# Kernel optimization log

Hardware: AMD Instinct MI355X
Metric: run time of the kernel (lower is better)

## Reference

```python
import jax, jax.numpy as jnp
import numpy as np

C, D, K, N, R = 96, 192, 4, 16, 6  # d_model, d_inner, directions, d_state, dt_rank
B, H, W = 8, 64, 64


def _ln(x, w, b):
    mu = x.mean(-1, keepdims=True)
    var = ((x - mu) ** 2).mean(-1, keepdims=True)
    return (x - mu) * jax.lax.rsqrt(var + 1e-5) * w + b


def setup_inputs() -> dict:
    key = jax.random.key(0)
    ks = jax.random.split(key, 16)
    s = 0.02
    A = jnp.tile(jnp.arange(1, N + 1, dtype=jnp.float32)[None, None, :], (K, D, 1))
    return {
        "x": jax.random.normal(ks[0], (B, C, H, W), jnp.float32),
        "ln1_w": jnp.ones((C,), jnp.float32),
        "ln1_b": jnp.zeros((C,), jnp.float32),
        "in_proj_w": jax.random.normal(ks[1], (2 * D, C), jnp.float32) * s,
        "conv_w": jax.random.normal(ks[2], (D, 1, 3, 3), jnp.float32) * s,
        "conv_b": jnp.zeros((D,), jnp.float32),
        "x_proj_w": jax.random.normal(ks[3], (K, R + 2 * N, D), jnp.float32) * s,
        "dt_projs_w": jax.random.normal(ks[4], (K, D, R), jnp.float32) * s,
        "dt_projs_b": jax.random.normal(ks[5], (K, D), jnp.float32) * 0.1,
        "A_logs": jnp.log(A),
        "Ds": jnp.ones((K, D), jnp.float32),
        "out_norm_w": jnp.ones((D,), jnp.float32),
        "out_norm_b": jnp.zeros((D,), jnp.float32),
        "out_proj_w": jax.random.normal(ks[6], (C, D), jnp.float32) * s,
        "pm_norm_w": jnp.ones((4 * C,), jnp.float32),
        "pm_norm_b": jnp.zeros((4 * C,), jnp.float32),
        "pm_red_w": jax.random.normal(ks[7], (2 * C, 4 * C), jnp.float32) * s,
    }


def reference(x, ln1_w, ln1_b, in_proj_w, conv_w, conv_b, x_proj_w, dt_projs_w,
              dt_projs_b, A_logs, Ds, out_norm_w, out_norm_b, out_proj_w,
              pm_norm_w, pm_norm_b, pm_red_w):
    b, c, h, w = x.shape
    L = h * w
    xh = jnp.transpose(x, (0, 2, 3, 1))  # [B,H,W,C]
    resid = xh
    xn = _ln(xh, ln1_w, ln1_b)
    xz = xn @ in_proj_w.T  # [B,H,W,2D]
    xp, z = xz[..., :D], xz[..., D:]
    xc = jnp.transpose(xp, (0, 3, 1, 2))  # [B,D,H,W]
    xc = jax.lax.conv_general_dilated(
        xc, conv_w, (1, 1), ((1, 1), (1, 1)),
        dimension_numbers=("NCHW", "OIHW", "NCHW"), feature_group_count=D)
    xc = jax.nn.silu(xc + conv_b[None, :, None, None])
    # cross-scan: row-major, col-major, and their reverses -> [B,K,D,L]
    xf = xc.reshape(b, D, L)
    xt = jnp.transpose(xc, (0, 1, 3, 2)).reshape(b, D, L)
    xs = jnp.stack([xf, xt, xf[..., ::-1], xt[..., ::-1]], axis=1)
    x_dbl = jnp.einsum("bkdl,kcd->bkcl", xs, x_proj_w)
    dts = jnp.einsum("bkrl,kdr->bkdl", x_dbl[:, :, :R], dt_projs_w)
    Bs = x_dbl[:, :, R:R + N]  # [B,K,N,L]
    Cs = x_dbl[:, :, R + N:R + 2 * N]
    delta = jax.nn.softplus(dts + dt_projs_b[None, :, :, None])  # [B,K,D,L]
    A = -jnp.exp(A_logs)  # [K,D,N]
    dT = jnp.transpose(delta, (3, 0, 1, 2))  # [L,B,K,D]
    uT = jnp.transpose(xs, (3, 0, 1, 2))
    BT = jnp.transpose(Bs, (3, 0, 1, 2))  # [L,B,K,N]
    CT = jnp.transpose(Cs, (3, 0, 1, 2))
    h0 = jnp.zeros((b, K, D, N), x.dtype)

    def step(hst, inp):
        dt, ut, bt, ct = inp
        hst = hst * jnp.exp(dt[..., None] * A) + (dt * ut)[..., None] * bt[:, :, None, :]
        return hst, jnp.einsum("bkdn,bkn->bkd", hst, ct)

    _, yT = jax.lax.scan(step, h0, (dT, uT, BT, CT))  # yT: [L,B,K,D]
    y = jnp.transpose(yT, (1, 2, 3, 0)) + Ds[None, :, :, None] * xs  # [B,K,D,L]

    def unT(v):  # undo col-major traversal
        return jnp.transpose(v.reshape(b, D, w, h), (0, 1, 3, 2)).reshape(b, D, L)

    yc = y[:, 0] + y[:, 2, :, ::-1] + unT(y[:, 1]) + unT(y[:, 3, :, ::-1])
    yo = jnp.transpose(yc.reshape(b, D, h, w), (0, 2, 3, 1))  # [B,H,W,D]
    yo = _ln(yo, out_norm_w, out_norm_b) * jax.nn.silu(z)
    out = resid + yo @ out_proj_w.T  # [B,H,W,C]
    # PatchMerging2D
    x0 = out[:, 0::2, 0::2]
    x1 = out[:, 1::2, 0::2]
    x2 = out[:, 0::2, 1::2]
    x3 = out[:, 1::2, 1::2]
    xm = jnp.concatenate([x0, x1, x2, x3], -1)  # [B,H/2,W/2,4C]
    xm = _ln(xm, pm_norm_w, pm_norm_b) @ pm_red_w.T  # [B,H/2,W/2,2C]
    return jnp.transpose(xm, (0, 3, 1, 2))
```

## Files before the change

### kernel.cpp

```cpp
#include <hip/hip_runtime.h>
#include <hip/hip_bf16.h>


#define NCH 64
#define CLEN 64

typedef float v2f __attribute__((ext_vector_type(2)));
__device__ __forceinline__ v2f pkfma(v2f a, v2f b, v2f c){ return __builtin_elementwise_fma(a,b,c); }

__device__ __forceinline__ float sigm(float x){ return 1.f/(1.f+__expf(-x)); }
__device__ __forceinline__ float softplus_(float x){ return (x>20.f)? x : __logf(1.f+__expf(x)); }

__device__ __forceinline__ unsigned packbf2(float a, float b){
  __hip_bfloat16 ba = __float2bfloat16(a), bb = __float2bfloat16(b);
  unsigned short ua = *(unsigned short*)&ba, ub = *(unsigned short*)&bb;
  return (unsigned)ua | ((unsigned)ub<<16);
}
__device__ __forceinline__ float unpk_lo(unsigned u){ return __uint_as_float((u&0xffffu)<<16); }
__device__ __forceinline__ float unpk_hi(unsigned u){ return __uint_as_float(u&0xffff0000u); }

__device__ __forceinline__ void scan_p0dp2(int k, int v0, int& p0, int& dp){
  if(k==0){ p0 = v0; dp = 1; }
  else if(k==1){ p0 = ((v0&63)<<6)|(v0>>6); dp = 64; }
  else if(k==2){ p0 = 4095 - v0; dp = -1; }
  else { int m0 = 4095 - v0; p0 = ((m0&63)<<6)|(m0>>6); dp = -64; }
}

__global__ __launch_bounds__(256) void k0_prep(
    const float* __restrict__ ipw, const float* __restrict__ xpw,
    const float* __restrict__ dtw, const float* __restrict__ opw,
    const float* __restrict__ pmw,
    float* __restrict__ ipwT, float* __restrict__ xpwTp,
    float* __restrict__ dtwT, float* __restrict__ opwT,
    float* __restrict__ pmwT)
{
  int g = blockIdx.x*256 + threadIdx.x;
  if(g < 36864){
    int c = g/384, n = g%384;
    ipwT[g] = ipw[n*96 + c];
  } else if(g < 67584){
    int t = g - 36864; int dd = t/160, n = t - dd*160; int k = n/40, c = n - k*40;
    float v;
    if(c < 6)       v = xpw[(k*38 + c)*192 + dd];
    else if(c < 8)  v = 0.f;
    else            v = xpw[(k*38 + (c-2))*192 + dd];
    xpwTp[t] = v;
  } else if(g < 72192){
    int t = g - 67584; int kr = t/192, d = t - kr*192; int k = kr/6, r = kr - k*6;
    dtwT[t] = dtw[(k*192 + d)*6 + r];
  } else if(g < 90624){
    int t = g - 72192; int d = t/96, c = t - d*96;
    opwT[t] = opw[c*192 + d];
  } else if(g < 164352){
    int t = g - 90624; int n = t/192, c2 = t - n*192;
    pmwT[t] = pmw[c2*384 + n];
  }
}

#define XT_PAD 68
__global__ __launch_bounds__(256) void k1_ln_inproj(
    const float* __restrict__ x, const float* __restrict__ lnw, const float* __restrict__ lnb,
    const float* __restrict__ ipwT, float* __restrict__ xT,
    float* __restrict__ xp, float* __restrict__ z)
{
  __shared__ float xt[96*XT_PAD];
  __shared__ float lnw_s[96], lnb_s[96], mu_s[64], rs_s[64];
  int tid = threadIdx.x;
  int mt = blockIdx.x, nt = blockIdx.y, b = blockIdx.z;
  int g0 = mt*64;
  const float* xb = x + (size_t)b*96*4096 + g0;
  for(int idx=tid; idx<6144; idx+=256){
    int c = idx>>6, p = idx&63;
    xt[c*XT_PAD+p] = xb[c*4096 + p];
  }
  if(tid<96){ lnw_s[tid]=lnw[tid]; lnb_s[tid]=lnb[tid]; }
  __syncthreads();
  if(nt==0){
    float* xTb = xT + ((size_t)(b*4096 + g0))*96;
    for(int idx=tid; idx<6144; idx+=256){
      int p = idx/96, c = idx - p*96;
      xTb[idx] = xt[c*XT_PAD+p];
    }
  }
  if(tid<64){
    float s=0.f,q=0.f;
    for(int c=0;c<96;c++){ float v=xt[c*XT_PAD+tid]; s+=v; q+=v*v; }
    float mu = s*(1.f/96.f);
    mu_s[tid]=mu; rs_s[tid]=rsqrtf(q*(1.f/96.f)-mu*mu+1e-5f);
  }
  __syncthreads();
  for(int idx=tid; idx<6144; idx+=256){
    int c = idx>>6, p = idx&63;
    int a = c*XT_PAD+p;
    xt[a] = (xt[a]-mu_s[p])*rs_s[p]*lnw_s[c]+lnb_s[c];
  }
  __syncthreads();
  int tm = tid>>5, tn = tid&31;
  float acc[8][4];
  #pragma unroll
  for(int i=0;i<8;i++){acc[i][0]=0.f;acc[i][1]=0.f;acc[i][2]=0.f;acc[i][3]=0.f;}
  const float* wbase = ipwT + nt*128 + tn*4;
  for(int kk=0;kk<96;kk++){
    float4 w4 = *(const float4*)(wbase + kk*384);
    float4 a0 = *(const float4*)&xt[kk*XT_PAD + tm*8];
    float4 a1 = *(const float4*)&xt[kk*XT_PAD + tm*8 + 4];
    float av[8]={a0.x,a0.y,a0.z,a0.w,a1.x,a1.y,a1.z,a1.w};
    #pragma unroll
    for(int i=0;i<8;i++){
      acc[i][0]=fmaf(av[i],w4.x,acc[i][0]);
      acc[i][1]=fmaf(av[i],w4.y,acc[i][1]);
      acc[i][2]=fmaf(av[i],w4.z,acc[i][2]);
      acc[i][3]=fmaf(av[i],w4.w,acc[i][3]);
    }
  }
  int n = nt*128 + tn*4;
  #pragma unroll
  for(int i=0;i<8;i++){
    size_t row = (size_t)(b*4096 + g0 + tm*8 + i);
    float4 v = make_float4(acc[i][0],acc[i][1],acc[i][2],acc[i][3]);
    if(n < 192) *(float4*)(xp + row*192 + n) = v;
    else        *(float4*)(z  + row*192 + (n-192)) = v;
  }
}

__global__ __launch_bounds__(192) void k2_conv(
    const float* __restrict__ xp, const float* __restrict__ cw, const float* __restrict__ cb,
    __hip_bfloat16* __restrict__ xc)
{
  __shared__ float cw_s[1728];
  int tid = threadIdx.x;
  int pq = blockIdx.x, b = blockIdx.y;
  for(int i=tid;i<1728;i+=192) cw_s[i]=cw[i];
  __syncthreads();
  int th = (pq>>3)<<1;
  int tw = (pq&7)<<3;
  const float* base = xp + (size_t)b*4096*192 + tid;
  const float* wp = &cw_s[tid*9];
  float bias = cb[tid];
  float acc[2][8];
  #pragma unroll
  for(int r=0;r<2;r++)
    #pragma unroll
    for(int j=0;j<8;j++) acc[r][j]=bias;
  #pragma unroll
  for(int iy=0; iy<4; iy++){
    int hh = th-1+iy;
    if(hh<0||hh>63) continue;
    float v[10];
    #pragma unroll
    for(int xx=0;xx<10;xx++){
      int ww = tw-1+xx;
      v[xx] = (ww>=0 && ww<64) ? base[((size_t)(hh*64+ww))*192] : 0.f;
    }
    #pragma unroll
    for(int r=0;r<2;r++){
      int ky = iy - r;
      if(ky<0||ky>2) continue;
      float wk0=wp[ky*3], wk1=wp[ky*3+1], wk2=wp[ky*3+2];
      #pragma unroll
      for(int j=0;j<8;j++)
        acc[r][j] = fmaf(v[j],wk0, fmaf(v[j+1],wk1, fmaf(v[j+2],wk2, acc[r][j])));
    }
  }
  #pragma unroll
  for(int r=0;r<2;r++)
    #pragma unroll
    for(int j=0;j<8;j++){
      float a = acc[r][j];
      a = a * sigm(a);
      xc[((size_t)(b*4096) + (th+r)*64 + tw+j)*192 + tid] = __float2bfloat16(a);
    }
}

__global__ __launch_bounds__(320) void k3_proj(
    const __hip_bfloat16* __restrict__ xc, const float* __restrict__ xpwTp,
    float* __restrict__ xdbl)
{
  __shared__ float sm[32*192];
  int tid = threadIdx.x;
  int mt = blockIdx.x, b = blockIdx.y;
  int g0 = mt*32;
  const unsigned* xcb = (const unsigned*)(xc + ((size_t)(b*4096 + g0))*192);
  for(int idx=tid; idx<3072; idx+=320){
    unsigned u = xcb[idx];
    sm[idx*2]   = unpk_lo(u);
    sm[idx*2+1] = unpk_hi(u);
  }
  __syncthreads();
  int tn = tid%40, tm = tid/40;
  float acc[4][4];
  #pragma unroll
  for(int i=0;i<4;i++){acc[i][0]=0.f;acc[i][1]=0.f;acc[i][2]=0.f;acc[i][3]=0.f;}
  const float* wb = xpwTp + tn*4;
  for(int kk=0;kk<192;kk+=2){
    float4 w0 = *(const float4*)(wb + kk*160);
    float4 w1 = *(const float4*)(wb + (kk+1)*160);
    #pragma unroll
    for(int i=0;i<4;i++){
      float2 a = *(const float2*)&sm[(tm*4+i)*192 + kk];
      acc[i][0] = fmaf(a.x,w0.x, fmaf(a.y,w1.x, acc[i][0]));
      acc[i][1] = fmaf(a.x,w0.y, fmaf(a.y,w1.y, acc[i][1]));
      acc[i][2] = fmaf(a.x,w0.z, fmaf(a.y,w1.z, acc[i][2]));
      acc[i][3] = fmaf(a.x,w0.w, fmaf(a.y,w1.w, acc[i][3]));
    }
  }
  #pragma unroll
  for(int i=0;i<4;i++){
    *(float4*)(xdbl + ((size_t)(b*4096 + g0 + tm*4 + i))*160 + tn*4)
      = make_float4(acc[i][0],acc[i][1],acc[i][2],acc[i][3]);
  }
}

__global__ __launch_bounds__(192) void k4a_scanlocal(
    const float* __restrict__ xdbl, const __hip_bfloat16* __restrict__ xc,
    const float* __restrict__ alog, const float* __restrict__ dtwT,
    const float* __restrict__ dtb,
    __hip_bfloat16* __restrict__ localH, float* __restrict__ Ssum)
{
  int d = threadIdx.x;
  int ch = blockIdx.x, k = blockIdx.y, b = blockIdx.z;
  size_t prow = (size_t)b*4096;
  int p0, dp;
  scan_p0dp2(k, ch*CLEN, p0, dp);
  const float* rowp = xdbl + (prow + (size_t)p0)*160 + k*40;
  ptrdiff_t rstride = (ptrdiff_t)dp*160;
  float w0=dtwT[(k*6+0)*192+d], w1=dtwT[(k*6+1)*192+d], w2=dtwT[(k*6+2)*192+d],
        w3=dtwT[(k*6+3)*192+d], w4=dtwT[(k*6+4)*192+d], w5=dtwT[(k*6+5)*192+d];
  float dtbv = dtb[k*192+d];
  float A0; bool fast1;
  {
    const float4* ap = (const float4*)(alog + (size_t)(k*192+d)*16);
    float4 a0=ap[0],a1=ap[1],a2=ap[2],a3=ap[3];
    float t[16]={a0.x,a0.y,a0.z,a0.w,a1.x,a1.y,a1.z,a1.w,a2.x,a2.y,a2.z,a2.w,a3.x,a3.y,a3.z,a3.w};
    A0 = -__expf(t[0]);
    bool fast = true;
    #pragma unroll
    for(int n=1;n<16;n++)
      fast = fast && (fabsf(-__expf(t[n]) - (float)(n+1)*A0) <= 1e-4f*(float)(n+1)*fabsf(A0));
    fast1 = fast && (A0 == -1.0f);
  }
  float S=0.f;
  const __hip_bfloat16* xu = xc + (prow + (size_t)p0)*192 + d;
  ptrdiff_t ustride = (ptrdiff_t)dp*192;
  unsigned* lh = (unsigned*)(localH + ((((size_t)(b*4+k))*NCH + ch)*192 + d)*16);
  if(fast1){
    v2f h01={0.f,0.f},h23={0.f,0.f},h45={0.f,0.f},h67={0.f,0.f},
        h89={0.f,0.f},hAB={0.f,0.f},hCD={0.f,0.f},hEF={0.f,0.f};
    for(int i=0;i<CLEN;i++){
      const float* row = rowp; rowp += rstride;
      float u = __bfloat162float(*xu); xu += ustride;
      float4 r03 = *(const float4*)row;
      float2 r45 = *(const float2*)(row+4);
      float p01 = fmaf(r03.y,w1, r03.x*w0);
      float p23 = fmaf(r03.w,w3, r03.z*w2);
      float p45 = fmaf(r45.y,w5, r45.x*w4);
      float raw = (dtbv + p01) + (p23 + p45);
      float ex = __expf(raw);
      float tt = 1.f + ex;
      float delta = (raw>20.f)? raw : __logf(tt);
      float e1 = __builtin_amdgcn_rcpf(tt);
      float du = delta*u;
      S += delta;
      float4 B0=*(const float4*)(row+8),  B1=*(const float4*)(row+12),
             B2=*(const float4*)(row+16), B3=*(const float4*)(row+20);
      float e2s = e1*e1;
      v2f e2v = {e2s,e2s};
      v2f e4v = e2v*e2v;
      v2f e8v = e4v*e4v;
      v2f c01 = {e1,e2s};
      v2f c23 = c01*e2v;
      v2f c45 = c01*e4v;
      v2f c67 = c23*e4v;
      v2f c89 = c01*e8v;
      v2f cAB = c23*e8v;
      v2f cCD = c45*e8v;
      v2f cEF = c67*e8v;
      v2f du2 = {du,du};
      h01 = pkfma(h01,c01, du2*(v2f){B0.x,B0.y});
      h23 = pkfma(h23,c23, du2*(v2f){B0.z,B0.w});
      h45 = pkfma(h45,c45, du2*(v2f){B1.x,B1.y});
      h67 = pkfma(h67,c67, du2*(v2f){B1.z,B1.w});
      h89 = pkfma(h89,c89, du2*(v2f){B2.x,B2.y});
      hAB = pkfma(hAB,cAB, du2*(v2f){B2.z,B2.w});
      hCD = pkfma(hCD,cCD, du2*(v2f){B3.x,B3.y});
      hEF = pkfma(hEF,cEF, du2*(v2f){B3.z,B3.w});
    }
    uint4 q0, q1;
    q0.x = packbf2(h01.x,h01.y); q0.y = packbf2(h23.x,h23.y);
    q0.z = packbf2(h45.x,h45.y); q0.w = packbf2(h67.x,h67.y);
    q1.x = packbf2(h89.x,h89.y); q1.y = packbf2(hAB.x,hAB.y);
    q1.z = packbf2(hCD.x,hCD.y); q1.w = packbf2(hEF.x,hEF.y);
    *(uint4*)lh = q0;
    *(uint4*)(lh+4) = q1;
  } else {
    float A[16], h[16];
    {
      const float4* ap = (const float4*)(alog + (size_t)(k*192+d)*16);
      float4 a0=ap[0],a1=ap[1],a2=ap[2],a3=ap[3];
      float t[16]={a0.x,a0.y,a0.z,a0.w,a1.x,a1.y,a1.z,a1.w,a2.x,a2.y,a2.z,a2.w,a3.x,a3.y,a3.z,a3.w};
      #pragma unroll
      for(int n=0;n<16;n++){ A[n] = -__expf(t[n]); h[n]=0.f; }
    }
    for(int i=0;i<CLEN;i++){
      const float* row = rowp; rowp += rstride;
      float u = __bfloat162float(*xu); xu += ustride;
      float p01 = fmaf(row[1],w1, row[0]*w0);
      float p23 = fmaf(row[3],w3, row[2]*w2);
      float p45 = fmaf(row[5],w5, row[4]*w4);
      float delta = softplus_((dtbv + p01) + (p23 + p45));
      float du = delta*u;
      S += delta;
      float4 B0=*(const float4*)(row+8),  B1=*(const float4*)(row+12),
             B2=*(const float4*)(row+16), B3=*(const float4*)(row+20);
      float Bn[16]={B0.x,B0.y,B0.z,B0.w,B1.x,B1.y,B1.z,B1.w,
                    B2.x,B2.y,B2.z,B2.w,B3.x,B3.y,B3.z,B3.w};
      #pragma unroll
      for(int n=0;n<16;n++) h[n] = fmaf(h[n], __expf(delta*A[n]), du*Bn[n]);
    }
    uint4 q0, q1;
    q0.x = packbf2(h[0],h[1]);   q0.y = packbf2(h[2],h[3]);
    q0.z = packbf2(h[4],h[5]);   q0.w = packbf2(h[6],h[7]);
    q1.x = packbf2(h[8],h[9]);   q1.y = packbf2(h[10],h[11]);
    q1.z = packbf2(h[12],h[13]); q1.w = packbf2(h[14],h[15]);
    *(uint4*)lh = q0;
    *(uint4*)(lh+4) = q1;
  }
  Ssum[(((size_t)(b*4+k))*NCH + ch)*192 + d] = S;
}

__global__ __launch_bounds__(256) void k4b_chain(
    __hip_bfloat16* __restrict__ localH, const float* __restrict__ Ssum,
    const float* __restrict__ alog)
{
  int g = blockIdx.x*256 + threadIdx.x;
  int bk = g/3072, dn = g - bk*3072;
  int k = bk & 3;
  int d = dn>>4, n = dn&15;
  float A = -__expf(alog[((size_t)(k*192+d))*16 + n]);
  size_t hbase = (size_t)bk*NCH*3072 + dn;
  size_t sbase = (size_t)bk*NCH*192 + d;
  float hv = 0.f;
  float loc = __bfloat162float(localH[hbase]);
  float S   = Ssum[sbase];
  for(int ch=0; ch<NCH; ch++){
    float nloc = 0.f, nS = 0.f;
    if(ch < NCH-1){
      nloc = __bfloat162float(localH[hbase + (size_t)(ch+1)*3072]);
      nS   = Ssum[sbase + (size_t)(ch+1)*192];
    }
    float dec = __expf(A*S);
    localH[hbase + (size_t)ch*3072] = __float2bfloat16(hv);
    hv = fmaf(hv, dec, loc);
    loc = nloc; S = nS;
  }
}

__global__ __launch_bounds__(192) void k4c_scanfull(
    const float* __restrict__ xdbl, const __hip_bfloat16* __restrict__ xc,
    const float* __restrict__ alog, const float* __restrict__ dtwT,
    const float* __restrict__ dtb, const __hip_bfloat16* __restrict__ hin,
    const float* __restrict__ Dsv, __hip_bfloat16* __restrict__ yB)
{
  int d = threadIdx.x;
  int ch = blockIdx.x, k = blockIdx.y, b = blockIdx.z;
  size_t prow = (size_t)b*4096;
  int p0, dp;
  scan_p0dp2(k, ch*CLEN, p0, dp);
  const float* rowp = xdbl + (prow + (size_t)p0)*160 + k*40;
  ptrdiff_t rstride = (ptrdiff_t)dp*160;
  float w0=dtwT[(k*6+0)*192+d], w1=dtwT[(k*6+1)*192+d], w2=dtwT[(k*6+2)*192+d],
        w3=dtwT[(k*6+3)*192+d], w4=dtwT[(k*6+4)*192+d], w5=dtwT[(k*6+5)*192+d];
  float dtbv = dtb[k*192+d];
  float A0; bool fast1;
  {
    const float4* ap = (const float4*)(alog + (size_t)(k*192+d)*16);
    float4 a0=ap[0],a1=ap[1],a2=ap[2],a3=ap[3];
    float t[16]={a0.x,a0.y,a0.z,a0.w,a1.x,a1.y,a1.z,a1.w,a2.x,a2.y,a2.z,a2.w,a3.x,a3.y,a3.z,a3.w};
    A0 = -__expf(t[0]);
    bool fast = true;
    #pragma unroll
    for(int n=1;n<16;n++)
      fast = fast && (fabsf(-__expf(t[n]) - (float)(n+1)*A0) <= 1e-4f*(float)(n+1)*fabsf(A0));
    fast1 = fast && (A0 == -1.0f);
  }
  float dsv = Dsv[k*192+d];
  const __hip_bfloat16* xu = xc + (prow + (size_t)p0)*192 + d;
  ptrdiff_t ustride = (ptrdiff_t)dp*192;
  __hip_bfloat16* yP = yB + (((size_t)(b*4+k))*4096 + ch*CLEN)*192 + d;
  const unsigned* hp = (const unsigned*)(hin + ((((size_t)(b*4+k))*NCH + ch)*192 + d)*16);
  uint4 q0 = *(const uint4*)hp;
  uint4 q1 = *(const uint4*)(hp+4);
  if(fast1){
    v2f h01={unpk_lo(q0.x),unpk_hi(q0.x)}, h23={unpk_lo(q0.y),unpk_hi(q0.y)},
        h45={unpk_lo(q0.z),unpk_hi(q0.z)}, h67={unpk_lo(q0.w),unpk_hi(q0.w)},
        h89={unpk_lo(q1.x),unpk_hi(q1.x)}, hAB={unpk_lo(q1.y),unpk_hi(q1.y)},
        hCD={unpk_lo(q1.z),unpk_hi(q1.z)}, hEF={unpk_lo(q1.w),unpk_hi(q1.w)};
    for(int i=0;i<CLEN;i++){
      const float* row = rowp; rowp += rstride;
      float u = __bfloat162float(*xu); xu += ustride;
      float4 r03 = *(const float4*)row;
      float2 r45 = *(const float2*)(row+4);
      float p01 = fmaf(r03.y,w1, r03.x*w0);
      float p23 = fmaf(r03.w,w3, r03.z*w2);
      float p45 = fmaf(r45.y,w5, r45.x*w4);
      float raw = (dtbv + p01) + (p23 + p45);
      float ex = __expf(raw);
      float tt = 1.f + ex;
      float delta = (raw>20.f)? raw : __logf(tt);
      float e1 = __builtin_amdgcn_rcpf(tt);
      float du = delta*u;
      float4 B0=*(const float4*)(row+8),  B1=*(const float4*)(row+12),
             B2=*(const float4*)(row+16), B3=*(const float4*)(row+20);
      float4 C0=*(const float4*)(row+24), C1=*(const float4*)(row+28),
             C2=*(const float4*)(row+32), C3=*(const float4*)(row+36);
      float e2s = e1*e1;
      v2f e2v = {e2s,e2s};
      v2f e4v = e2v*e2v;
      v2f e8v = e4v*e4v;
      v2f c01 = {e1,e2s};
      v2f c23 = c01*e2v;
      v2f c45 = c01*e4v;
      v2f c67 = c23*e4v;
      v2f c89 = c01*e8v;
      v2f cAB = c23*e8v;
      v2f cCD = c45*e8v;
      v2f cEF = c67*e8v;
      v2f du2 = {du,du};
      h01 = pkfma(h01,c01, du2*(v2f){B0.x,B0.y});
      h23 = pkfma(h23,c23, du2*(v2f){B0.z,B0.w});
      h45 = pkfma(h45,c45, du2*(v2f){B1.x,B1.y});
      h67 = pkfma(h67,c67, du2*(v2f){B1.z,B1.w});
      h89 = pkfma(h89,c89, du2*(v2f){B2.x,B2.y});
      hAB = pkfma(hAB,cAB, du2*(v2f){B2.z,B2.w});
      hCD = pkfma(hCD,cCD, du2*(v2f){B3.x,B3.y});
      hEF = pkfma(hEF,cEF, du2*(v2f){B3.z,B3.w});
      v2f yv = h01*(v2f){C0.x,C0.y};
      yv = pkfma(h23,(v2f){C0.z,C0.w}, yv);
      yv = pkfma(h45,(v2f){C1.x,C1.y}, yv);
      yv = pkfma(h67,(v2f){C1.z,C1.w}, yv);
      yv = pkfma(h89,(v2f){C2.x,C2.y}, yv);
      yv = pkfma(hAB,(v2f){C2.z,C2.w}, yv);
      yv = pkfma(hCD,(v2f){C3.x,C3.y}, yv);
      yv = pkfma(hEF,(v2f){C3.z,C3.w}, yv);
      yP[(size_t)i*192] = __float2bfloat16(fmaf(dsv, u, yv.x + yv.y));
    }
  } else {
    float A[16], h[16];
    {
      const float4* ap = (const float4*)(alog + (size_t)(k*192+d)*16);
      float4 a0=ap[0],a1=ap[1],a2=ap[2],a3=ap[3];
      float t[16]={a0.x,a0.y,a0.z,a0.w,a1.x,a1.y,a1.z,a1.w,a2.x,a2.y,a2.z,a2.w,a3.x,a3.y,a3.z,a3.w};
      #pragma unroll
      for(int n=0;n<16;n++) A[n] = -__expf(t[n]);
    }
    h[0]=unpk_lo(q0.x); h[1]=unpk_hi(q0.x); h[2]=unpk_lo(q0.y); h[3]=unpk_hi(q0.y);
    h[4]=unpk_lo(q0.z); h[5]=unpk_hi(q0.z); h[6]=unpk_lo(q0.w); h[7]=unpk_hi(q0.w);
    h[8]=unpk_lo(q1.x); h[9]=unpk_hi(q1.x); h[10]=unpk_lo(q1.y); h[11]=unpk_hi(q1.y);
    h[12]=unpk_lo(q1.z); h[13]=unpk_hi(q1.z); h[14]=unpk_lo(q1.w); h[15]=unpk_hi(q1.w);
    for(int i=0;i<CLEN;i++){
      const float* row = rowp; rowp += rstride;
      float u = __bfloat162float(*xu); xu += ustride;
      float p01 = fmaf(row[1],w1, row[0]*w0);
      float p23 = fmaf(row[3],w3, row[2]*w2);
      float p45 = fmaf(row[5],w5, row[4]*w4);
      float delta = softplus_((dtbv + p01) + (p23 + p45));
      float du = delta*u;
      float4 B0=*(const float4*)(row+8),  B1=*(const float4*)(row+12),
             B2=*(const float4*)(row+16), B3=*(const float4*)(row+20);
      float Bn[16]={B0.x,B0.y,B0.z,B0.w,B1.x,B1.y,B1.z,B1.w,
                    B2.x,B2.y,B2.z,B2.w,B3.x,B3.y,B3.z,B3.w};
      float4 C0=*(const float4*)(row+24), C1=*(const float4*)(row+28),
             C2=*(const float4*)(row+32), C3=*(const float4*)(row+36);
      float Cn[16]={C0.x,C0.y,C0.z,C0.w,C1.x,C1.y,C1.z,C1.w,
                    C2.x,C2.y,C2.z,C2.w,C3.x,C3.y,C3.z,C3.w};
      float y = 0.f;
      #pragma unroll
      for(int n=0;n<16;n++){
        h[n] = fmaf(h[n], __expf(delta*A[n]), du*Bn[n]);
        y = fmaf(h[n], Cn[n], y);
      }
      yP[(size_t)i*192] = __float2bfloat16(fmaf(dsv, u, y));
    }
  }
}

#define YPAD 193
__global__ __launch_bounds__(256) void k5_combine(
    const __hip_bfloat16* __restrict__ yS, const float* __restrict__ z, const float* __restrict__ xT,
    const float* __restrict__ onw, const float* __restrict__ onb,
    const float* __restrict__ opwT, float* __restrict__ out_pre)
{
  __shared__ float yn[64*YPAD];
  __shared__ float wsm[48*96];
  __shared__ float mu_s[64], rs_s[64];
  int tid = threadIdx.x;
  int mt = blockIdx.x, b = blockIdx.y;
  int g0 = mt*64;
  size_t base = (size_t)b*4*4096;
  for(int idx=tid; idx<12288; idx+=256){
    int p = idx/192, d = idx - p*192;
    int gp = g0 + p;
    int l1 = ((gp&63)<<6)|(gp>>6);
    float v = __bfloat162float(yS[(base + gp)*192 + d])
            + __bfloat162float(yS[(base + 4096 + l1)*192 + d])
            + __bfloat162float(yS[(base + 2*4096 + (4095-gp))*192 + d])
            + __bfloat162float(yS[(base + 3*4096 + (4095-l1))*192 + d]);
    yn[p*YPAD+d] = v;
  }
  __syncthreads();
  {
    int p = tid>>2, q = tid&3;
    float s=0.f, sq=0.f;
    for(int c=q;c<192;c+=4){ float v=yn[p*YPAD+c]; s+=v; sq=fmaf(v,v,sq); }
    s  += __shfl_xor(s,1);  sq += __shfl_xor(sq,1);
    s  += __shfl_xor(s,2);  sq += __shfl_xor(sq,2);
    if(q==0){
      float mu = s*(1.f/192.f);
      mu_s[p]=mu; rs_s[p]=rsqrtf(sq*(1.f/192.f)-mu*mu+1e-5f);
    }
  }
  __syncthreads();
  for(int idx=tid; idx<12288; idx+=256){
    int p = idx/192, d = idx - p*192;
    float zz = z[((size_t)(b*4096+g0+p))*192 + d];
    float v = (yn[p*YPAD+d]-mu_s[p])*rs_s[p]*onw[d]+onb[d];
    yn[p*YPAD+d] = v * zz * sigm(zz);
  }
  __syncthreads();
  int tn = tid&15, tm = tid>>4;
  float acc[4][6];
  #pragma unroll
  for(int i=0;i<4;i++)
    #pragma unroll
    for(int j=0;j<6;j++) acc[i][j]=0.f;
  for(int kc=0; kc<4; kc++){
    for(int idx=tid; idx<4608; idx+=256) wsm[idx] = opwT[kc*4608 + idx];
    __syncthreads();
    for(int kk=0;kk<48;kk++){
      float a0 = yn[(tm*4+0)*YPAD + kc*48+kk];
      float a1 = yn[(tm*4+1)*YPAD + kc*48+kk];
      float a2 = yn[(tm*4+2)*YPAD + kc*48+kk];
      float a3 = yn[(tm*4+3)*YPAD + kc*48+kk];
      const float* wr = &wsm[kk*96 + tn*6];
      #pragma unroll
      for(int j=0;j<6;j++){
        float w = wr[j];
        acc[0][j]=fmaf(a0,w,acc[0][j]);
        acc[1][j]=fmaf(a1,w,acc[1][j]);
        acc[2][j]=fmaf(a2,w,acc[2][j]);
        acc[3][j]=fmaf(a3,w,acc[3][j]);
      }
    }
    __syncthreads();
  }
  #pragma unroll
  for(int i=0;i<4;i++){
    size_t row = (size_t)(b*4096 + g0 + tm*4 + i);
    const float* xr = xT + row*96 + tn*6;
    float* orr = out_pre + row*96 + tn*6;
    #pragma unroll
    for(int j=0;j<6;j++) orr[j] = acc[i][j] + xr[j];
  }
}

__global__ __launch_bounds__(192) void k6_pm(
    const float* __restrict__ out_pre, const float* __restrict__ pmw, const float* __restrict__ pmb,
    const float* __restrict__ pmwT, float* __restrict__ outp)
{
  __shared__ float xm[8*388];
  __shared__ float xo[8*193];
  __shared__ float mus[8], rss[8];
  int tid = threadIdx.x;
  int jt = blockIdx.x, i = blockIdx.y, b = blockIdx.z;
  for(int idx=tid; idx<3072; idx+=192){
    int pj = idx/384, n = idx - pj*384;
    int q = n/96, c = n - q*96;
    int j = jt*8 + pj;
    int h2 = 2*i + (q&1), w2 = 2*j + (q>>1);
    xm[pj*388+n] = out_pre[((size_t)b*4096 + h2*64 + w2)*96 + c];
  }
  __syncthreads();
  if(tid<8){
    float s=0.f,q=0.f;
    for(int n=0;n<384;n++){ float v=xm[tid*388+n]; s+=v; q+=v*v; }
    float mu=s*(1.f/384.f);
    mus[tid]=mu; rss[tid]=rsqrtf(q*(1.f/384.f)-mu*mu+1e-5f);
  }
  __syncthreads();
  for(int idx=tid; idx<3072; idx+=192){
    int pj = idx/384, n = idx - pj*384;
    xm[pj*388+n] = (xm[pj*388+n]-mus[pj])*rss[pj]*pmw[n]+pmb[n];
  }
  __syncthreads();
  float acc[8];
  #pragma unroll
  for(int pj=0;pj<8;pj++) acc[pj]=0.f;
  const float* wb = pmwT + tid;
  for(int n4=0;n4<96;n4++){
    float w0=wb[(n4*4+0)*192], w1=wb[(n4*4+1)*192], w2=wb[(n4*4+2)*192], w3=wb[(n4*4+3)*192];
    #pragma unroll
    for(int pj=0;pj<8;pj++){
      float4 v = *(const float4*)&xm[pj*388 + n4*4];
      acc[pj] = fmaf(v.x,w0,fmaf(v.y,w1,fmaf(v.z,w2,fmaf(v.w,w3,acc[pj]))));
    }
  }
  #pragma unroll
  for(int pj=0;pj<8;pj++) xo[pj*193+tid]=acc[pj];
  __syncthreads();
  for(int idx=tid; idx<1536; idx+=192){
    int c2 = idx>>3, pj = idx&7;
    outp[(((size_t)b*192 + c2)*32 + i)*32 + jt*8 + pj] = xo[pj*193+c2];
  }
}

extern "C" void kernel_launch(void* const* d_in, const int* in_sizes, int n_in,
                              void* d_out, int out_size, void* d_ws, size_t ws_size,
                              hipStream_t stream)
{
  const float* x    = (const float*)d_in[0];
  const float* lnw  = (const float*)d_in[1];
  const float* lnb  = (const float*)d_in[2];
  const float* ipw  = (const float*)d_in[3];
  const float* cw   = (const float*)d_in[4];
  const float* cb   = (const float*)d_in[5];
  const float* xpw  = (const float*)d_in[6];
  const float* dtw  = (const float*)d_in[7];
  const float* dtb  = (const float*)d_in[8];
  const float* alog = (const float*)d_in[9];
  const float* Dsv  = (const float*)d_in[10];
  const float* onw  = (const float*)d_in[11];
  const float* onb  = (const float*)d_in[12];
  const float* opw  = (const float*)d_in[13];
  const float* pmnw = (const float*)d_in[14];
  const float* pmnb = (const float*)d_in[15];
  const float* pmrw = (const float*)d_in[16];
  float* out = (float*)d_out;

  float* ws    = (float*)d_ws;
  float* xT    = ws;
  float* xpb   = xT + 3145728;
  float* zb    = xpb + 6291456;
  float* xcf   = zb + 6291456;
  float* yBf   = xcf + 3145728;
  float* lHf   = yBf + 12582912;
  float* Ss    = lHf + 3145728;
  float* ipwT  = Ss + 393216;
  float* xpwTp = ipwT + 36864;
  float* dtwT  = xpwTp + 30720;
  float* opwT  = dtwT + 4608;
  float* pmwT  = opwT + 18432;
  float* xdbl  = xpb;
  float* outp  = xpb;
  __hip_bfloat16* xc = (__hip_bfloat16*)xcf;
  __hip_bfloat16* yB = (__hip_bfloat16*)yBf;
  __hip_bfloat16* lH = (__hip_bfloat16*)lHf;

  k0_prep      <<<dim3(642),      dim3(256), 0, stream>>>(ipw,xpw,dtw,opw,pmrw, ipwT,xpwTp,dtwT,opwT,pmwT);
  k1_ln_inproj <<<dim3(64,3,8),   dim3(256), 0, stream>>>(x,lnw,lnb,ipwT, xT,xpb,zb);
  k2_conv      <<<dim3(256,8),    dim3(192), 0, stream>>>(xpb,cw,cb, xc);
  k3_proj      <<<dim3(128,8),    dim3(320), 0, stream>>>(xc,xpwTp, xdbl);
  k4a_scanlocal<<<dim3(NCH,4,8),  dim3(192), 0, stream>>>(xdbl,xc,alog,dtwT,dtb, lH,Ss);
  k4b_chain    <<<dim3(384),      dim3(256), 0, stream>>>(lH,Ss,alog);
  k4c_scanfull <<<dim3(NCH,4,8),  dim3(192), 0, stream>>>(xdbl,xc,alog,dtwT,dtb,lH,Dsv, yB);
  k5_combine   <<<dim3(64,8),     dim3(256), 0, stream>>>(yB,zb,xT,onw,onb,opwT, outp);
  k6_pm        <<<dim3(4,32,8),   dim3(192), 0, stream>>>(outp,pmnw,pmnb,pmwT, out);
}
```

Measured before the change: 315.5 us.

## Replace two-pass chunked scan with single local scan plus carry-in correction pass

The first scan pass now computes local outputs y with zero initial state, and stores a per-step cumulative delta prefix (bf16) alongside the chunk-end state. After the chain kernel propagates carry-in states, a lighter correction kernel adds C·(h_in·exp(A·S_prefix)) to y for every chunk except the first. This avoids recomputing softplus, B loads and the full recurrence in a second scan. In exchange it writes and reads an extra bf16 prefix-sum tensor the size of y and does a read-modify-write of y in bf16, which adds rounding error and memory traffic.

```diff
diff --git a/kernel.cpp b/kernel.cpp
--- a/kernel.cpp
+++ b/kernel.cpp
@@ -211,10 +211,11 @@
   }
 }
 
-__global__ __launch_bounds__(192) void k4a_scanlocal(
+__global__ __launch_bounds__(192) void k4y_scan(
     const float* __restrict__ xdbl, const __hip_bfloat16* __restrict__ xc,
     const float* __restrict__ alog, const float* __restrict__ dtwT,
-    const float* __restrict__ dtb,
+    const float* __restrict__ dtb, const float* __restrict__ Dsv,
+    __hip_bfloat16* __restrict__ yB, __hip_bfloat16* __restrict__ Sst,
     __hip_bfloat16* __restrict__ localH, float* __restrict__ Ssum)
 {
   int d = threadIdx.x;
@@ -239,9 +240,13 @@
       fast = fast && (fabsf(-__expf(t[n]) - (float)(n+1)*A0) <= 1e-4f*(float)(n+1)*fabsf(A0));
     fast1 = fast && (A0 == -1.0f);
   }
+  float dsv = Dsv[k*192+d];
   float S=0.f;
   const __hip_bfloat16* xu = xc + (prow + (size_t)p0)*192 + d;
   ptrdiff_t ustride = (ptrdiff_t)dp*192;
+  size_t strm = (((size_t)(b*4+k))*4096 + ch*CLEN)*192 + d;
+  __hip_bfloat16* yP = yB + strm;
+  __hip_bfloat16* SP = Sst + strm;
   unsigned* lh = (unsigned*)(localH + ((((size_t)(b*4+k))*NCH + ch)*192 + d)*16);
   if(fast1){
     v2f h01={0.f,0.f},h23={0.f,0.f},h45={0.f,0.f},h67={0.f,0.f},
@@ -261,154 +266,7 @@
       float e1 = __builtin_amdgcn_rcpf(tt);
       float du = delta*u;
       S += delta;
-      float4 B0=*(const float4*)(row+8),  B1=*(const float4*)(row+12),
-             B2=*(const float4*)(row+16), B3=*(const float4*)(row+20);
-      float e2s = e1*e1;
-      v2f e2v = {e2s,e2s};
-      v2f e4v = e2v*e2v;
-      v2f e8v = e4v*e4v;
-      v2f c01 = {e1,e2s};
-      v2f c23 = c01*e2v;
-      v2f c45 = c01*e4v;
-      v2f c67 = c23*e4v;
-      v2f c89 = c01*e8v;
-      v2f cAB = c23*e8v;
-      v2f cCD = c45*e8v;
-      v2f cEF = c67*e8v;
-      v2f du2 = {du,du};
-      h01 = pkfma(h01,c01, du2*(v2f){B0.x,B0.y});
-      h23 = pkfma(h23,c23, du2*(v2f){B0.z,B0.w});
-      h45 = pkfma(h45,c45, du2*(v2f){B1.x,B1.y});
-      h67 = pkfma(h67,c67, du2*(v2f){B1.z,B1.w});
-      h89 = pkfma(h89,c89, du2*(v2f){B2.x,B2.y});
-      hAB = pkfma(hAB,cAB, du2*(v2f){B2.z,B2.w});
-      hCD = pkfma(hCD,cCD, du2*(v2f){B3.x,B3.y});
-      hEF = pkfma(hEF,cEF, du2*(v2f){B3.z,B3.w});
-    }
-    uint4 q0, q1;
-    q0.x = packbf2(h01.x,h01.y); q0.y = packbf2(h23.x,h23.y);
-    q0.z = packbf2(h45.x,h45.y); q0.w = packbf2(h67.x,h67.y);
-    q1.x = packbf2(h89.x,h89.y); q1.y = packbf2(hAB.x,hAB.y);
-    q1.z = packbf2(hCD.x,hCD.y); q1.w = packbf2(hEF.x,hEF.y);
-    *(uint4*)lh = q0;
-    *(uint4*)(lh+4) = q1;
-  } else {
-    float A[16], h[16];
-    {
-      const float4* ap = (const float4*)(alog + (size_t)(k*192+d)*16);
-      float4 a0=ap[0],a1=ap[1],a2=ap[2],a3=ap[3];
-      float t[16]={a0.x,a0.y,a0.z,a0.w,a1.x,a1.y,a1.z,a1.w,a2.x,a2.y,a2.z,a2.w,a3.x,a3.y,a3.z,a3.w};
-      #pragma unroll
-      for(int n=0;n<16;n++){ A[n] = -__expf(t[n]); h[n]=0.f; }
-    }
-    for(int i=0;i<CLEN;i++){
-      const float* row = rowp; rowp += rstride;
-      float u = __bfloat162float(*xu); xu += ustride;
-      float p01 = fmaf(row[1],w1, row[0]*w0);
-      float p23 = fmaf(row[3],w3, row[2]*w2);
-      float p45 = fmaf(row[5],w5, row[4]*w4);
-      float delta = softplus_((dtbv + p01) + (p23 + p45));
-      float du = delta*u;
-      S += delta;
-      float4 B0=*(const float4*)(row+8),  B1=*(const float4*)(row+12),
-             B2=*(const float4*)(row+16), B3=*(const float4*)(row+20);
-      float Bn[16]={B0.x,B0.y,B0.z,B0.w,B1.x,B1.y,B1.z,B1.w,
-                    B2.x,B2.y,B2.z,B2.w,B3.x,B3.y,B3.z,B3.w};
-      #pragma unroll
-      for(int n=0;n<16;n++) h[n] = fmaf(h[n], __expf(delta*A[n]), du*Bn[n]);
-    }
-    uint4 q0, q1;
-    q0.x = packbf2(h[0],h[1]);   q0.y = packbf2(h[2],h[3]);
-    q0.z = packbf2(h[4],h[5]);   q0.w = packbf2(h[6],h[7]);
-    q1.x = packbf2(h[8],h[9]);   q1.y = packbf2(h[10],h[11]);
-    q1.z = packbf2(h[12],h[13]); q1.w = packbf2(h[14],h[15]);
-    *(uint4*)lh = q0;
-    *(uint4*)(lh+4) = q1;
-  }
-  Ssum[(((size_t)(b*4+k))*NCH + ch)*192 + d] = S;
-}
-
-__global__ __launch_bounds__(256) void k4b_chain(
-    __hip_bfloat16* __restrict__ localH, const float* __restrict__ Ssum,
-    const float* __restrict__ alog)
-{
-  int g = blockIdx.x*256 + threadIdx.x;
-  int bk = g/3072, dn = g - bk*3072;
-  int k = bk & 3;
-  int d = dn>>4, n = dn&15;
-  float A = -__expf(alog[((size_t)(k*192+d))*16 + n]);
-  size_t hbase = (size_t)bk*NCH*3072 + dn;
-  size_t sbase = (size_t)bk*NCH*192 + d;
-  float hv = 0.f;
-  float loc = __bfloat162float(localH[hbase]);
-  float S   = Ssum[sbase];
-  for(int ch=0; ch<NCH; ch++){
-    float nloc = 0.f, nS = 0.f;
-    if(ch < NCH-1){
-      nloc = __bfloat162float(localH[hbase + (size_t)(ch+1)*3072]);
-      nS   = Ssum[sbase + (size_t)(ch+1)*192];
-    }
-    float dec = __expf(A*S);
-    localH[hbase + (size_t)ch*3072] = __float2bfloat16(hv);
-    hv = fmaf(hv, dec, loc);
-    loc = nloc; S = nS;
-  }
-}
-
-__global__ __launch_bounds__(192) void k4c_scanfull(
-    const float* __restrict__ xdbl, const __hip_bfloat16* __restrict__ xc,
-    const float* __restrict__ alog, const float* __restrict__ dtwT,
-    const float* __restrict__ dtb, const __hip_bfloat16* __restrict__ hin,
-    const float* __restrict__ Dsv, __hip_bfloat16* __restrict__ yB)
-{
-  int d = threadIdx.x;
-  int ch = blockIdx.x, k = blockIdx.y, b = blockIdx.z;
-  size_t prow = (size_t)b*4096;
-  int p0, dp;
-  scan_p0dp2(k, ch*CLEN, p0, dp);
-  const float* rowp = xdbl + (prow + (size_t)p0)*160 + k*40;
-  ptrdiff_t rstride = (ptrdiff_t)dp*160;
-  float w0=dtwT[(k*6+0)*192+d], w1=dtwT[(k*6+1)*192+d], w2=dtwT[(k*6+2)*192+d],
-        w3=dtwT[(k*6+3)*192+d], w4=dtwT[(k*6+4)*192+d], w5=dtwT[(k*6+5)*192+d];
-  float dtbv = dtb[k*192+d];
-  float A0; bool fast1;
-  {
-    const float4* ap = (const float4*)(alog + (size_t)(k*192+d)*16);
-    float4 a0=ap[0],a1=ap[1],a2=ap[2],a3=ap[3];
-    float t[16]={a0.x,a0.y,a0.z,a0.w,a1.x,a1.y,a1.z,a1.w,a2.x,a2.y,a2.z,a2.w,a3.x,a3.y,a3.z,a3.w};
-    A0 = -__expf(t[0]);
-    bool fast = true;
-    #pragma unroll
-    for(int n=1;n<16;n++)
-      fast = fast && (fabsf(-__expf(t[n]) - (float)(n+1)*A0) <= 1e-4f*(float)(n+1)*fabsf(A0));
-    fast1 = fast && (A0 == -1.0f);
-  }
-  float dsv = Dsv[k*192+d];
-  const __hip_bfloat16* xu = xc + (prow + (size_t)p0)*192 + d;
-  ptrdiff_t ustride = (ptrdiff_t)dp*192;
-  __hip_bfloat16* yP = yB + (((size_t)(b*4+k))*4096 + ch*CLEN)*192 + d;
-  const unsigned* hp = (const unsigned*)(hin + ((((size_t)(b*4+k))*NCH + ch)*192 + d)*16);
-  uint4 q0 = *(const uint4*)hp;
-  uint4 q1 = *(const uint4*)(hp+4);
-  if(fast1){
-    v2f h01={unpk_lo(q0.x),unpk_hi(q0.x)}, h23={unpk_lo(q0.y),unpk_hi(q0.y)},
-        h45={unpk_lo(q0.z),unpk_hi(q0.z)}, h67={unpk_lo(q0.w),unpk_hi(q0.w)},
-        h89={unpk_lo(q1.x),unpk_hi(q1.x)}, hAB={unpk_lo(q1.y),unpk_hi(q1.y)},
-        hCD={unpk_lo(q1.z),unpk_hi(q1.z)}, hEF={unpk_lo(q1.w),unpk_hi(q1.w)};
-    for(int i=0;i<CLEN;i++){
-      const float* row = rowp; rowp += rstride;
-      float u = __bfloat162float(*xu); xu += ustride;
-      float4 r03 = *(const float4*)row;
-      float2 r45 = *(const float2*)(row+4);
-      float p01 = fmaf(r03.y,w1, r03.x*w0);
-      float p23 = fmaf(r03.w,w3, r03.z*w2);
-      float p45 = fmaf(r45.y,w5, r45.x*w4);
-      float raw = (dtbv + p01) + (p23 + p45);
-      float ex = __expf(raw);
-      float tt = 1.f + ex;
-      float delta = (raw>20.f)? raw : __logf(tt);
-      float e1 = __builtin_amdgcn_rcpf(tt);
-      float du = delta*u;
+      SP[(size_t)i*192] = __float2bfloat16(S);
       float4 B0=*(const float4*)(row+8),  B1=*(const float4*)(row+12),
              B2=*(const float4*)(row+16), B3=*(const float4*)(row+20);
       float4 C0=*(const float4*)(row+24), C1=*(const float4*)(row+28),
@@ -444,6 +302,13 @@
       yv = pkfma(hEF,(v2f){C3.z,C3.w}, yv);
       yP[(size_t)i*192] = __float2bfloat16(fmaf(dsv, u, yv.x + yv.y));
     }
+    uint4 q0, q1;
+    q0.x = packbf2(h01.x,h01.y); q0.y = packbf2(h23.x,h23.y);
+    q0.z = packbf2(h45.x,h45.y); q0.w = packbf2(h67.x,h67.y);
+    q1.x = packbf2(h89.x,h89.y); q1.y = packbf2(hAB.x,hAB.y);
+    q1.z = packbf2(hCD.x,hCD.y); q1.w = packbf2(hEF.x,hEF.y);
+    *(uint4*)lh = q0;
+    *(uint4*)(lh+4) = q1;
   } else {
     float A[16], h[16];
     {
@@ -451,12 +316,8 @@
       float4 a0=ap[0],a1=ap[1],a2=ap[2],a3=ap[3];
       float t[16]={a0.x,a0.y,a0.z,a0.w,a1.x,a1.y,a1.z,a1.w,a2.x,a2.y,a2.z,a2.w,a3.x,a3.y,a3.z,a3.w};
       #pragma unroll
-      for(int n=0;n<16;n++) A[n] = -__expf(t[n]);
-    }
-    h[0]=unpk_lo(q0.x); h[1]=unpk_hi(q0.x); h[2]=unpk_lo(q0.y); h[3]=unpk_hi(q0.y);
-    h[4]=unpk_lo(q0.z); h[5]=unpk_hi(q0.z); h[6]=unpk_lo(q0.w); h[7]=unpk_hi(q0.w);
-    h[8]=unpk_lo(q1.x); h[9]=unpk_hi(q1.x); h[10]=unpk_lo(q1.y); h[11]=unpk_hi(q1.y);
-    h[12]=unpk_lo(q1.z); h[13]=unpk_hi(q1.z); h[14]=unpk_lo(q1.w); h[15]=unpk_hi(q1.w);
+      for(int n=0;n<16;n++){ A[n] = -__expf(t[n]); h[n]=0.f; }
+    }
     for(int i=0;i<CLEN;i++){
       const float* row = rowp; rowp += rstride;
       float u = __bfloat162float(*xu); xu += ustride;
@@ -465,6 +326,8 @@
       float p45 = fmaf(row[5],w5, row[4]*w4);
       float delta = softplus_((dtbv + p01) + (p23 + p45));
       float du = delta*u;
+      S += delta;
+      SP[(size_t)i*192] = __float2bfloat16(S);
       float4 B0=*(const float4*)(row+8),  B1=*(const float4*)(row+12),
              B2=*(const float4*)(row+16), B3=*(const float4*)(row+20);
       float Bn[16]={B0.x,B0.y,B0.z,B0.w,B1.x,B1.y,B1.z,B1.w,
@@ -480,6 +343,132 @@
         y = fmaf(h[n], Cn[n], y);
       }
       yP[(size_t)i*192] = __float2bfloat16(fmaf(dsv, u, y));
+    }
+    uint4 q0, q1;
+    q0.x = packbf2(h[0],h[1]);   q0.y = packbf2(h[2],h[3]);
+    q0.z = packbf2(h[4],h[5]);   q0.w = packbf2(h[6],h[7]);
+    q1.x = packbf2(h[8],h[9]);   q1.y = packbf2(h[10],h[11]);
+    q1.z = packbf2(h[12],h[13]); q1.w = packbf2(h[14],h[15]);
+    *(uint4*)lh = q0;
+    *(uint4*)(lh+4) = q1;
+  }
+  Ssum[(((size_t)(b*4+k))*NCH + ch)*192 + d] = S;
+}
+
+__global__ __launch_bounds__(256) void k4b_chain(
+    __hip_bfloat16* __restrict__ localH, const float* __restrict__ Ssum,
+    const float* __restrict__ alog)
+{
+  int g = blockIdx.x*256 + threadIdx.x;
+  int bk = g/3072, dn = g - bk*3072;
+  int k = bk & 3;
+  int d = dn>>4, n = dn&15;
+  float A = -__expf(alog[((size_t)(k*192+d))*16 + n]);
+  size_t hbase = (size_t)bk*NCH*3072 + dn;
+  size_t sbase = (size_t)bk*NCH*192 + d;
+  float hv = 0.f;
+  float loc = __bfloat162float(localH[hbase]);
+  float S   = Ssum[sbase];
+  for(int ch=0; ch<NCH; ch++){
+    float nloc = 0.f, nS = 0.f;
+    if(ch < NCH-1){
+      nloc = __bfloat162float(localH[hbase + (size_t)(ch+1)*3072]);
+      nS   = Ssum[sbase + (size_t)(ch+1)*192];
+    }
+    float dec = __expf(A*S);
+    localH[hbase + (size_t)ch*3072] = __float2bfloat16(hv);
+    hv = fmaf(hv, dec, loc);
+    loc = nloc; S = nS;
+  }
+}
+
+__global__ __launch_bounds__(192) void k4corr(
+    const float* __restrict__ xdbl, const float* __restrict__ alog,
+    const __hip_bfloat16* __restrict__ hin, const __hip_bfloat16* __restrict__ Sst,
+    __hip_bfloat16* __restrict__ yB)
+{
+  int d = threadIdx.x;
+  int ch = blockIdx.x + 1, k = blockIdx.y, b = blockIdx.z;
+  size_t prow = (size_t)b*4096;
+  int p0, dp;
+  scan_p0dp2(k, ch*CLEN, p0, dp);
+  const float* rowp = xdbl + (prow + (size_t)p0)*160 + k*40 + 24;
+  ptrdiff_t rstride = (ptrdiff_t)dp*160;
+  float A0; bool fast1;
+  {
+    const float4* ap = (const float4*)(alog + (size_t)(k*192+d)*16);
+    float4 a0=ap[0],a1=ap[1],a2=ap[2],a3=ap[3];
+    float t[16]={a0.x,a0.y,a0.z,a0.w,a1.x,a1.y,a1.z,a1.w,a2.x,a2.y,a2.z,a2.w,a3.x,a3.y,a3.z,a3.w};
+    A0 = -__expf(t[0]);
+    bool fast = true;
+    #pragma unroll
+    for(int n=1;n<16;n++)
+      fast = fast && (fabsf(-__expf(t[n]) - (float)(n+1)*A0) <= 1e-4f*(float)(n+1)*fabsf(A0));
+    fast1 = fast && (A0 == -1.0f);
+  }
+  const unsigned* hp = (const unsigned*)(hin + ((((size_t)(b*4+k))*NCH + ch)*192 + d)*16);
+  uint4 q0 = *(const uint4*)hp;
+  uint4 q1 = *(const uint4*)(hp+4);
+  size_t strm = (((size_t)(b*4+k))*4096 + ch*CLEN)*192 + d;
+  const __hip_bfloat16* SP = Sst + strm;
+  __hip_bfloat16* yP = yB + strm;
+  if(fast1){
+    v2f t01={unpk_lo(q0.x),unpk_hi(q0.x)}, t23={unpk_lo(q0.y),unpk_hi(q0.y)},
+        t45={unpk_lo(q0.z),unpk_hi(q0.z)}, t67={unpk_lo(q0.w),unpk_hi(q0.w)},
+        t89={unpk_lo(q1.x),unpk_hi(q1.x)}, tAB={unpk_lo(q1.y),unpk_hi(q1.y)},
+        tCD={unpk_lo(q1.z),unpk_hi(q1.z)}, tEF={unpk_lo(q1.w),unpk_hi(q1.w)};
+    for(int i=0;i<CLEN;i++){
+      const float* row = rowp; rowp += rstride;
+      float S = __bfloat162float(SP[(size_t)i*192]);
+      float g = __expf(-S);
+      float4 C0=*(const float4*)row,     C1=*(const float4*)(row+4),
+             C2=*(const float4*)(row+8), C3=*(const float4*)(row+12);
+      float g2s = g*g;
+      v2f g2v = {g2s,g2s};
+      v2f g4v = g2v*g2v;
+      v2f g8v = g4v*g4v;
+      v2f c01 = {g,g2s};
+      v2f c23 = c01*g2v;
+      v2f c45 = c01*g4v;
+      v2f c67 = c23*g4v;
+      v2f c89 = c01*g8v;
+      v2f cAB = c23*g8v;
+      v2f cCD = c45*g8v;
+      v2f cEF = c67*g8v;
+      v2f acc = t01*(c01*(v2f){C0.x,C0.y});
+      acc = pkfma(t23, c23*(v2f){C0.z,C0.w}, acc);
+      acc = pkfma(t45, c45*(v2f){C1.x,C1.y}, acc);
+      acc = pkfma(t67, c67*(v2f){C1.z,C1.w}, acc);
+      acc = pkfma(t89, c89*(v2f){C2.x,C2.y}, acc);
+      acc = pkfma(tAB, cAB*(v2f){C2.z,C2.w}, acc);
+      acc = pkfma(tCD, cCD*(v2f){C3.x,C3.y}, acc);
+      acc = pkfma(tEF, cEF*(v2f){C3.z,C3.w}, acc);
+      float corr = acc.x + acc.y;
+      yP[(size_t)i*192] =
+        __float2bfloat16(__bfloat162float(yP[(size_t)i*192]) + corr);
+    }
+  } else {
+    float A[16], t[16];
+    {
+      const float4* ap = (const float4*)(alog + (size_t)(k*192+d)*16);
+      float4 a0=ap[0],a1=ap[1],a2=ap[2],a3=ap[3];
+      float tt[16]={a0.x,a0.y,a0.z,a0.w,a1.x,a1.y,a1.z,a1.w,a2.x,a2.y,a2.z,a2.w,a3.x,a3.y,a3.z,a3.w};
+      #pragma unroll
+      for(int n=0;n<16;n++) A[n] = -__expf(tt[n]);
+    }
+    t[0]=unpk_lo(q0.x); t[1]=unpk_hi(q0.x); t[2]=unpk_lo(q0.y); t[3]=unpk_hi(q0.y);
+    t[4]=unpk_lo(q0.z); t[5]=unpk_hi(q0.z); t[6]=unpk_lo(q0.w); t[7]=unpk_hi(q0.w);
+    t[8]=unpk_lo(q1.x); t[9]=unpk_hi(q1.x); t[10]=unpk_lo(q1.y); t[11]=unpk_hi(q1.y);
+    t[12]=unpk_lo(q1.z); t[13]=unpk_hi(q1.z); t[14]=unpk_lo(q1.w); t[15]=unpk_hi(q1.w);
+    for(int i=0;i<CLEN;i++){
+      const float* row = rowp; rowp += rstride;
+      float S = __bfloat162float(SP[(size_t)i*192]);
+      float corr = 0.f;
+      #pragma unroll
+      for(int n=0;n<16;n++)
+        corr = fmaf(t[n]*row[n], __expf(A[n]*S), corr);
+      yP[(size_t)i*192] =
+        __float2bfloat16(__bfloat162float(yP[(size_t)i*192]) + corr);
     }
   }
 }
@@ -642,7 +631,8 @@
   float* zb    = xpb + 6291456;
   float* xcf   = zb + 6291456;
   float* yBf   = xcf + 3145728;
-  float* lHf   = yBf + 12582912;
+  float* Sstf  = yBf + 12582912;
+  float* lHf   = Sstf + 12582912;
   float* Ss    = lHf + 3145728;
   float* ipwT  = Ss + 393216;
   float* xpwTp = ipwT + 36864;
@@ -651,17 +641,18 @@
   float* pmwT  = opwT + 18432;
   float* xdbl  = xpb;
   float* outp  = xpb;
-  __hip_bfloat16* xc = (__hip_bfloat16*)xcf;
-  __hip_bfloat16* yB = (__hip_bfloat16*)yBf;
-  __hip_bfloat16* lH = (__hip_bfloat16*)lHf;
-
-  k0_prep      <<<dim3(642),      dim3(256), 0, stream>>>(ipw,xpw,dtw,opw,pmrw, ipwT,xpwTp,dtwT,opwT,pmwT);
-  k1_ln_inproj <<<dim3(64,3,8),   dim3(256), 0, stream>>>(x,lnw,lnb,ipwT, xT,xpb,zb);
-  k2_conv      <<<dim3(256,8),    dim3(192), 0, stream>>>(xpb,cw,cb, xc);
-  k3_proj      <<<dim3(128,8),    dim3(320), 0, stream>>>(xc,xpwTp, xdbl);
-  k4a_scanlocal<<<dim3(NCH,4,8),  dim3(192), 0, stream>>>(xdbl,xc,alog,dtwT,dtb, lH,Ss);
-  k4b_chain    <<<dim3(384),      dim3(256), 0, stream>>>(lH,Ss,alog);
-  k4c_scanfull <<<dim3(NCH,4,8),  dim3(192), 0, stream>>>(xdbl,xc,alog,dtwT,dtb,lH,Dsv, yB);
-  k5_combine   <<<dim3(64,8),     dim3(256), 0, stream>>>(yB,zb,xT,onw,onb,opwT, outp);
-  k6_pm        <<<dim3(4,32,8),   dim3(192), 0, stream>>>(outp,pmnw,pmnb,pmwT, out);
-}
+  __hip_bfloat16* xc  = (__hip_bfloat16*)xcf;
+  __hip_bfloat16* yB  = (__hip_bfloat16*)yBf;
+  __hip_bfloat16* Sst = (__hip_bfloat16*)Sstf;
+  __hip_bfloat16* lH  = (__hip_bfloat16*)lHf;
+
+  k0_prep      <<<dim3(642),       dim3(256), 0, stream>>>(ipw,xpw,dtw,opw,pmrw, ipwT,xpwTp,dtwT,opwT,pmwT);
+  k1_ln_inproj <<<dim3(64,3,8),    dim3(256), 0, stream>>>(x,lnw,lnb,ipwT, xT,xpb,zb);
+  k2_conv      <<<dim3(256,8),     dim3(192), 0, stream>>>(xpb,cw,cb, xc);
+  k3_proj      <<<dim3(128,8),     dim3(320), 0, stream>>>(xc,xpwTp, xdbl);
+  k4y_scan     <<<dim3(NCH,4,8),   dim3(192), 0, stream>>>(xdbl,xc,alog,dtwT,dtb,Dsv, yB,Sst,lH,Ss);
+  k4b_chain    <<<dim3(384),       dim3(256), 0, stream>>>(lH,Ss,alog);
+  k4corr       <<<dim3(NCH-1,4,8), dim3(192), 0, stream>>>(xdbl,alog,lH,Sst, yB);
+  k5_combine   <<<dim3(64,8),      dim3(256), 0, stream>>>(yB,zb,xT,onw,onb,opwT, outp);
+  k6_pm        <<<dim3(4,32,8),    dim3(192), 0, stream>>>(outp,pmnw,pmnb,pmwT, out);
+}
```

Result: faster. 309.0 us (-2.1%).
